# Kernel optimization log

Measured on AMD Instinct MI355X. Metric: run time of the kernel, lower is better.

The kernel has to match this reference:

```python
import jax, jax.numpy as jnp
import numpy as np

NUM_CHANNELS = 256
NUM_HEADS = 8
HEAD_DIM = NUM_CHANNELS // NUM_HEADS


def setup_inputs() -> dict:
    key = jax.random.key(0)
    k1, k2, k3, k4, k5 = jax.random.split(key, 5)
    C = NUM_CHANNELS
    s = 1.0 / np.sqrt(C)
    image = jax.random.normal(k1, (8, C, 32, 32), dtype=jnp.float32)
    # kqv_projection: Linear(C, 3C); mix_heads: Linear(C, C). Stored as [in, out].
    w_kqv = jax.random.uniform(k2, (C, 3 * C), minval=-s, maxval=s, dtype=jnp.float32)
    b_kqv = jax.random.uniform(k3, (3 * C,), minval=-s, maxval=s, dtype=jnp.float32)
    w_mix = jax.random.uniform(k4, (C, C), minval=-s, maxval=s, dtype=jnp.float32)
    b_mix = jax.random.uniform(k5, (C,), minval=-s, maxval=s, dtype=jnp.float32)
    return {"image": image, "w_kqv": w_kqv, "b_kqv": b_kqv, "w_mix": w_mix, "b_mix": b_mix}


def _masked_attention(seq, w_kqv, b_kqv, w_mix, b_mix):
    # seq: [N, T, C]
    N, T, C = seq.shape
    H, D = NUM_HEADS, HEAD_DIM
    projected = seq @ w_kqv + b_kqv            # [N, T, 3C]
    k, q, v = jnp.split(projected, 3, axis=-1)  # order: keys, queries, values
    # split heads -> [N, H, T, D]
    k = k.reshape(N, T, H, D).transpose(0, 2, 1, 3)
    q = q.reshape(N, T, H, D).transpose(0, 2, 1, 3)
    v = v.reshape(N, T, H, D).transpose(0, 2, 1, 3)
    logits = jnp.einsum('nhtd,nhsd->nhts', q, k) / jnp.sqrt(jnp.float32(D))
    causal = jnp.tril(jnp.ones((T, T), dtype=bool))
    logits = jnp.where(causal, logits, -jnp.inf)
    weights = jax.nn.softmax(logits, axis=-1)
    out = jnp.einsum('nhts,nhsd->nhtd', weights, v)  # [N, H, T, D]
    out = out.transpose(0, 2, 1, 3).reshape(N, T, C)  # combine heads
    return out @ w_mix + b_mix


def reference(image, w_kqv, b_kqv, w_mix, b_mix):
    N, C, Hh, Ww = image.shape
    seq = image.transpose(0, 2, 3, 1).reshape(N, Hh * Ww, C)
    attn = _masked_attention(seq, w_kqv, b_kqv, w_mix, b_mix)
    attn = attn.reshape(N, Hh, Ww, C).transpose(0, 3, 1, 2)
    return attn + image
```

## Files before the change

kernel.cpp:

```cpp
#include <hip/hip_runtime.h>
#include <math.h>

constexpr int NB  = 8;
constexpr int C   = 256;
constexpr int T   = 1024;
constexpr int NH  = 8;
constexpr int HD  = 32;
constexpr int C3  = 768;

constexpr float QSCALE = 0.25503489422229562f;

typedef __attribute__((ext_vector_type(8))) short bf16x8;
typedef __attribute__((ext_vector_type(4))) float f32x4;

__device__ inline short f2bf(float f) {
    unsigned u = __float_as_uint(f);
    u += 0x7FFF + ((u >> 16) & 1);
    return (short)(u >> 16);
}
__device__ inline short f2bf_trunc(float f) {
    return (short)(__float_as_uint(f) >> 16);
}

__global__ __launch_bounds__(256) void kqv_mfma(const float* __restrict__ image,
                                                const float* __restrict__ wkqv,
                                                const float* __restrict__ bkqv,
                                                short* __restrict__ Kb,
                                                short* __restrict__ Qb,
                                                short* __restrict__ Vtb) {
    __shared__ __align__(16) short As[128][40];
    __shared__ __align__(16) short Bs[64][40];
    const int tid = threadIdx.x;
    const int n0 = blockIdx.x * 64;
    const int m0 = blockIdx.y * 128;
    const int nb = m0 >> 10, t0 = m0 & 1023;
    const int wv = tid >> 6, lane = tid & 63;
    const int m = lane & 15, quad = lane >> 4;
    const int am = tid & 63, ak8 = (tid >> 6) * 8;

    const float* imgn = image + (size_t)nb * C * T;

    f32x4 acc[2][4];
    const f32x4 z = {0.f, 0.f, 0.f, 0.f};
    #pragma unroll
    for (int i = 0; i < 2; ++i)
        #pragma unroll
        for (int j = 0; j < 4; ++j) acc[i][j] = z;

    float fa[2][8], fb[8];
    #pragma unroll
    for (int i = 0; i < 8; ++i) {
        fa[0][i] = imgn[(size_t)(ak8 + i) * T + t0 + am];
        fa[1][i] = imgn[(size_t)(ak8 + i) * T + t0 + 64 + am];
        fb[i]    = wkqv[(size_t)(ak8 + i) * C3 + n0 + am];
    }

    for (int k0 = 0; k0 < C; k0 += 32) {
        __syncthreads();
        #pragma unroll
        for (int h2 = 0; h2 < 2; ++h2) {
            short4 lo = { f2bf(fa[h2][0]), f2bf(fa[h2][1]), f2bf(fa[h2][2]), f2bf(fa[h2][3]) };
            short4 hi = { f2bf(fa[h2][4]), f2bf(fa[h2][5]), f2bf(fa[h2][6]), f2bf(fa[h2][7]) };
            *(short4*)&As[64 * h2 + am][ak8]     = lo;
            *(short4*)&As[64 * h2 + am][ak8 + 4] = hi;
        }
        {
            short4 lo = { f2bf(fb[0]), f2bf(fb[1]), f2bf(fb[2]), f2bf(fb[3]) };
            short4 hi = { f2bf(fb[4]), f2bf(fb[5]), f2bf(fb[6]), f2bf(fb[7]) };
            *(short4*)&Bs[am][ak8]     = lo;
            *(short4*)&Bs[am][ak8 + 4] = hi;
        }
        if (k0 + 32 < C) {
            #pragma unroll
            for (int i = 0; i < 8; ++i) {
                fa[0][i] = imgn[(size_t)(k0 + 32 + ak8 + i) * T + t0 + am];
                fa[1][i] = imgn[(size_t)(k0 + 32 + ak8 + i) * T + t0 + 64 + am];
                fb[i]    = wkqv[(size_t)(k0 + 32 + ak8 + i) * C3 + n0 + am];
            }
        }
        __syncthreads();
        bf16x8 a[2], b[4];
        #pragma unroll
        for (int i = 0; i < 2; ++i) a[i] = *(const bf16x8*)&As[32 * wv + 16 * i + m][8 * quad];
        #pragma unroll
        for (int j = 0; j < 4; ++j) b[j] = *(const bf16x8*)&Bs[16 * j + m][8 * quad];
        #pragma unroll
        for (int i = 0; i < 2; ++i)
            #pragma unroll
            for (int j = 0; j < 4; ++j)
                acc[i][j] = __builtin_amdgcn_mfma_f32_16x16x32_bf16(a[i], b[j], acc[i][j], 0, 0, 0);
    }

    #pragma unroll
    for (int j = 0; j < 4; ++j) {
        int jj = n0 + 16 * j + m;
        int chunk = jj >> 8, hh = (jj >> 5) & 7, d = jj & 31;
        float bias = bkqv[jj];
        if (chunk < 2) {
            short* dst = (chunk == 0) ? Kb : Qb;
            float mul = (chunk == 1) ? QSCALE : 1.0f;
            size_t base = (size_t)(nb * NH + hh) * T * HD + d;
            #pragma unroll
            for (int i = 0; i < 2; ++i) {
                int t = t0 + 32 * wv + 16 * i + 4 * quad;
                #pragma unroll
                for (int r = 0; r < 4; ++r)
                    dst[base + (size_t)(t + r) * HD] = f2bf((acc[i][j][r] + bias) * mul);
            }
        } else {
            size_t base = (size_t)(nb * NH + hh) * (16 * 2048) + (size_t)d * 64;
            #pragma unroll
            for (int i = 0; i < 2; ++i) {
                #pragma unroll
                for (int r = 0; r < 4; ++r) {
                    int t = t0 + 32 * wv + 16 * i + 4 * quad + r;
                    Vtb[base + (size_t)(t >> 6) * 2048 + (t & 63)] = f2bf(acc[i][j][r] + bias);
                }
            }
        }
    }
}

__global__ __launch_bounds__(256) void attn_mfma(const short* __restrict__ Kb,
                                                 const short* __restrict__ Qb,
                                                 const short* __restrict__ Vtb,
                                                 short* __restrict__ attnb) {
    const int qb = (blockIdx.z & 4) ? 7 - blockIdx.x : blockIdx.x;
    const int h  = blockIdx.y;
    const int nb = blockIdx.z;
    const int tid  = threadIdx.x;
    const int wv   = tid >> 6;
    const int lane = tid & 63;
    const int m    = lane & 15;
    const int quad = lane >> 4;

    __shared__ __align__(16) short Ps[128][72];

    const int q0  = qb * 128;
    const int nst = 2 * qb + 2;
    const size_t hb = (size_t)(nb * NH + h) * T * HD;
    const short* Kp = Kb + hb;
    const short* Qp = Qb + hb;
    const short* Vp = Vtb + (size_t)(nb * NH + h) * (16 * 2048);
    const f32x4 z = {0.f, 0.f, 0.f, 0.f};

    bf16x8 aq[2];
    #pragma unroll
    for (int i = 0; i < 2; ++i)
        aq[i] = *(const bf16x8*)&Qp[(size_t)(q0 + 32 * wv + 16 * i + m) * HD + 8 * quad];

    bf16x8 bk[4], vb[2][2];
    #pragma unroll
    for (int j = 0; j < 4; ++j)
        bk[j] = *(const bf16x8*)&Kp[(size_t)(16 * j + m) * HD + 8 * quad];
    #pragma unroll
    for (int kc = 0; kc < 2; ++kc)
        #pragma unroll
        for (int hf = 0; hf < 2; ++hf)
            vb[kc][hf] = *(const bf16x8*)&Vp[(size_t)(16 * hf + m) * 64 + 32 * kc + 8 * quad];

    f32x4 O[2][2] = {{z, z}, {z, z}};
    float lp[2][4] = {};

    for (int st = 0; st < nst; ++st) {
        f32x4 S[2][4];
        #pragma unroll
        for (int i = 0; i < 2; ++i)
            #pragma unroll
            for (int j = 0; j < 4; ++j)
                S[i][j] = __builtin_amdgcn_mfma_f32_16x16x32_bf16(aq[i], bk[j], z, 0, 0, 0);

        if (st + 1 < nst) {
            #pragma unroll
            for (int j = 0; j < 4; ++j)
                bk[j] = *(const bf16x8*)&Kp[(size_t)((st + 1) * 64 + 16 * j + m) * HD + 8 * quad];
        }

        const bool msk = (st >= 2 * qb);
        const int s0 = st * 64;
        #pragma unroll
        for (int i = 0; i < 2; ++i) {
            const int qr_base = q0 + 32 * wv + 16 * i + 4 * quad;
            #pragma unroll
            for (int j = 0; j < 4; ++j) {
                const int sc = s0 + 16 * j + m;
                #pragma unroll
                for (int r = 0; r < 4; ++r) {
                    float e = __builtin_amdgcn_exp2f(S[i][j][r]);
                    if (msk && sc > qr_base + r) e = 0.f;
                    lp[i][r] += e;
                    Ps[32 * wv + 16 * i + 4 * quad + r][16 * j + m] = f2bf_trunc(e);
                }
            }
        }

        #pragma unroll
        for (int kc = 0; kc < 2; ++kc) {
            bf16x8 ap0 = *(const bf16x8*)&Ps[32 * wv + m][32 * kc + 8 * quad];
            bf16x8 ap1 = *(const bf16x8*)&Ps[32 * wv + 16 + m][32 * kc + 8 * quad];
            O[0][0] = __builtin_amdgcn_mfma_f32_16x16x32_bf16(ap0, vb[kc][0], O[0][0], 0, 0, 0);
            O[0][1] = __builtin_amdgcn_mfma_f32_16x16x32_bf16(ap0, vb[kc][1], O[0][1], 0, 0, 0);
            O[1][0] = __builtin_amdgcn_mfma_f32_16x16x32_bf16(ap1, vb[kc][0], O[1][0], 0, 0, 0);
            O[1][1] = __builtin_amdgcn_mfma_f32_16x16x32_bf16(ap1, vb[kc][1], O[1][1], 0, 0, 0);
        }

        if (st + 1 < nst) {
            const short* Vn = Vp + (size_t)(st + 1) * 2048;
            #pragma unroll
            for (int kc = 0; kc < 2; ++kc)
                #pragma unroll
                for (int hf = 0; hf < 2; ++hf)
                    vb[kc][hf] = *(const bf16x8*)&Vn[(size_t)(16 * hf + m) * 64 + 32 * kc + 8 * quad];
        }
    }

    #pragma unroll
    for (int i = 0; i < 2; ++i)
        #pragma unroll
        for (int r = 0; r < 4; ++r) {
            float l = lp[i][r];
            l += __shfl_xor(l, 1);
            l += __shfl_xor(l, 2);
            l += __shfl_xor(l, 4);
            l += __shfl_xor(l, 8);
            float inv = 1.f / l;
            int row = q0 + 32 * wv + 16 * i + 4 * quad + r;
            short* op = attnb + ((size_t)(nb * T + row)) * C + h * HD;
            op[m]      = f2bf(O[i][0][r] * inv);
            op[16 + m] = f2bf(O[i][1][r] * inv);
        }
}

__global__ __launch_bounds__(256) void mix_mfma(const short* __restrict__ attnb,
                                                const float* __restrict__ wmix,
                                                const float* __restrict__ bmix,
                                                const float* __restrict__ image,
                                                float* __restrict__ out) {
    __shared__ __align__(16) short Bs[64][264];
    const int tid = threadIdx.x;
    const int n0 = blockIdx.x * 64;
    const int m0 = blockIdx.y * 64;
    const int nb = m0 >> 10, t0 = m0 & 1023;
    const int wv = tid >> 6, lane = tid & 63;
    const int m = lane & 15, quad = lane >> 4;
    const int bn = tid & 63, bk8 = (tid >> 6) * 8;

    #pragma unroll
    for (int g = 0; g < 8; ++g) {
        int kk = bk8 + 32 * g;
        float fb[8];
        #pragma unroll
        for (int i = 0; i < 8; ++i)
            fb[i] = wmix[(size_t)(kk + i) * C + n0 + bn];
        short4 lo = { f2bf(fb[0]), f2bf(fb[1]), f2bf(fb[2]), f2bf(fb[3]) };
        short4 hi = { f2bf(fb[4]), f2bf(fb[5]), f2bf(fb[6]), f2bf(fb[7]) };
        *(short4*)&Bs[bn][kk]     = lo;
        *(short4*)&Bs[bn][kk + 4] = hi;
    }
    __syncthreads();

    f32x4 acc[4];
    const f32x4 z = {0.f, 0.f, 0.f, 0.f};
    #pragma unroll
    for (int j = 0; j < 4; ++j) acc[j] = z;

    #pragma unroll
    for (int k0 = 0; k0 < C; k0 += 32) {
        bf16x8 a = *(const bf16x8*)&attnb[(size_t)(m0 + 16 * wv + m) * C + k0 + 8 * quad];
        bf16x8 b[4];
        #pragma unroll
        for (int j = 0; j < 4; ++j) b[j] = *(const bf16x8*)&Bs[16 * j + m][k0 + 8 * quad];
        #pragma unroll
        for (int j = 0; j < 4; ++j)
            acc[j] = __builtin_amdgcn_mfma_f32_16x16x32_bf16(a, b[j], acc[j], 0, 0, 0);
    }

    const int tb = t0 + 16 * wv + 4 * quad;
    #pragma unroll
    for (int j = 0; j < 4; ++j) {
        int c = n0 + 16 * j + m;
        float bias = bmix[c];
        size_t o = (size_t)(nb * C + c) * T + tb;
        float4 img = *(const float4*)&image[o];
        float4 res = { acc[j][0] + bias + img.x,
                       acc[j][1] + bias + img.y,
                       acc[j][2] + bias + img.z,
                       acc[j][3] + bias + img.w };
        *(float4*)&out[o] = res;
    }
}

extern "C" void kernel_launch(void* const* d_in, const int* in_sizes, int n_in,
                              void* d_out, int out_size, void* d_ws, size_t ws_size,
                              hipStream_t stream) {
    const float* image = (const float*)d_in[0];
    const float* w_kqv = (const float*)d_in[1];
    const float* b_kqv = (const float*)d_in[2];
    const float* w_mix = (const float*)d_in[3];
    const float* b_mix = (const float*)d_in[4];
    float* out = (float*)d_out;

    short* Kb    = (short*)d_ws;
    short* Qb    = Kb  + (size_t)NB * NH * T * HD;
    short* Vtb   = Qb  + (size_t)NB * NH * T * HD;
    short* attnb = Vtb + (size_t)NB * NH * T * HD;

    kqv_mfma<<<dim3(C3 / 64, NB * T / 128), 256, 0, stream>>>(image, w_kqv, b_kqv, Kb, Qb, Vtb);
    attn_mfma<<<dim3(8, NH, NB), 256, 0, stream>>>(Kb, Qb, Vtb, attnb);
    mix_mfma<<<dim3(C / 64, NB * T / 64), 256, 0, stream>>>(attnb, w_mix, b_mix, image, out);
}
```

Measured before the change: 109.2 us.

## Pretranspose inputs to bf16 and use direct global-to-LDS loads in KQV GEMM

Adds a prep kernel that transposes the image and both weight matrices once and converts them to bf16. The KQV GEMM then streams 64-wide K tiles through global_load_lds into XOR-swizzled shared memory, and the mix GEMM copies pre-converted weights instead of converting them in every block. The attention loop is split so that only the last two diagonal tiles evaluate the causal mask. In exchange there is an extra launch plus an extra round trip of the image through memory, and the new KQV loop has no software prefetch.

```diff
diff --git a/kernel.cpp b/kernel.cpp
--- a/kernel.cpp
+++ b/kernel.cpp
@@ -22,23 +22,75 @@
     return (short)(__float_as_uint(f) >> 16);
 }
 
-__global__ __launch_bounds__(256) void kqv_mfma(const float* __restrict__ image,
-                                                const float* __restrict__ wkqv,
+__device__ __forceinline__ void gl16(const void* g, void* l) {
+    __builtin_amdgcn_global_load_lds(
+        (const __attribute__((address_space(1))) unsigned int*)g,
+        (__attribute__((address_space(3))) unsigned int*)l, 16, 0, 0);
+}
+
+__global__ __launch_bounds__(256) void prep_tc(const float* __restrict__ image,
+                                               const float* __restrict__ wkqv,
+                                               const float* __restrict__ wmix,
+                                               short* __restrict__ Xb,
+                                               short* __restrict__ Wkb,
+                                               short* __restrict__ Wmb) {
+    __shared__ float tile[64][65];
+    const int bid = blockIdx.x;
+    const int tid = threadIdx.x;
+    const float* src; short* dst;
+    int Cc, r0, c0;
+    if (bid < 512) {
+        const int nb = bid >> 6, t = bid & 63;
+        src = image + (size_t)nb * C * T;
+        dst = Xb + (size_t)nb * T * C;
+        Cc = T; r0 = (t & 3) * 64; c0 = (t >> 2) * 64;
+    } else if (bid < 560) {
+        const int t = bid - 512;
+        src = wkqv; dst = Wkb;
+        Cc = C3; r0 = (t & 3) * 64; c0 = (t >> 2) * 64;
+    } else {
+        const int t = bid - 560;
+        src = wmix; dst = Wmb;
+        Cc = C; r0 = (t & 3) * 64; c0 = (t >> 2) * 64;
+    }
+    const int lr = tid >> 4, lc = (tid & 15) * 4;
+    #pragma unroll
+    for (int p = 0; p < 4; ++p) {
+        float4 v = *(const float4*)&src[(size_t)(r0 + 16 * p + lr) * Cc + c0 + lc];
+        tile[16 * p + lr][lc + 0] = v.x;
+        tile[16 * p + lr][lc + 1] = v.y;
+        tile[16 * p + lr][lc + 2] = v.z;
+        tile[16 * p + lr][lc + 3] = v.w;
+    }
+    __syncthreads();
+    const int wc = tid >> 2, wr = (tid & 3) * 16;
+    bf16x8 v0, v1;
+    #pragma unroll
+    for (int e = 0; e < 8; ++e) v0[e] = f2bf(tile[wr + e][wc]);
+    #pragma unroll
+    for (int e = 0; e < 8; ++e) v1[e] = f2bf(tile[wr + 8 + e][wc]);
+    short* o = dst + (size_t)(c0 + wc) * C + r0 + wr;
+    *(bf16x8*)&o[0] = v0;
+    *(bf16x8*)&o[8] = v1;
+}
+
+__global__ __launch_bounds__(256) void kqv_mfma(const short* __restrict__ Xb,
+                                                const short* __restrict__ Wkb,
                                                 const float* __restrict__ bkqv,
                                                 short* __restrict__ Kb,
                                                 short* __restrict__ Qb,
                                                 short* __restrict__ Vtb) {
-    __shared__ __align__(16) short As[128][40];
-    __shared__ __align__(16) short Bs[64][40];
+    __shared__ __align__(16) short As[128 * 64];
+    __shared__ __align__(16) short Bs[64 * 64];
     const int tid = threadIdx.x;
     const int n0 = blockIdx.x * 64;
     const int m0 = blockIdx.y * 128;
     const int nb = m0 >> 10, t0 = m0 & 1023;
     const int wv = tid >> 6, lane = tid & 63;
     const int m = lane & 15, quad = lane >> 4;
-    const int am = tid & 63, ak8 = (tid >> 6) * 8;
-
-    const float* imgn = image + (size_t)nb * C * T;
+
+    const short* Xn = Xb + (size_t)nb * T * C + (size_t)t0 * C;
+    const short* Wn = Wkb + (size_t)n0 * C;
 
     f32x4 acc[2][4];
     const f32x4 z = {0.f, 0.f, 0.f, 0.f};
@@ -47,48 +99,45 @@
         #pragma unroll
         for (int j = 0; j < 4; ++j) acc[i][j] = z;
 
-    float fa[2][8], fb[8];
-    #pragma unroll
-    for (int i = 0; i < 8; ++i) {
-        fa[0][i] = imgn[(size_t)(ak8 + i) * T + t0 + am];
-        fa[1][i] = imgn[(size_t)(ak8 + i) * T + t0 + 64 + am];
-        fb[i]    = wkqv[(size_t)(ak8 + i) * C3 + n0 + am];
-    }
-
-    for (int k0 = 0; k0 < C; k0 += 32) {
+    const int sx = (m & 7) << 4;
+
+    for (int k0 = 0; k0 < C; k0 += 64) {
+        #pragma unroll
+        for (int p = 0; p < 4; ++p) {
+            const int o = p * 4096 + tid * 16;
+            const int row = o >> 7;
+            const int cb = (o & 127) ^ ((row & 7) << 4);
+            gl16(Xn + (size_t)row * C + k0 + (cb >> 1), (char*)As + o);
+        }
+        #pragma unroll
+        for (int p = 0; p < 2; ++p) {
+            const int o = p * 4096 + tid * 16;
+            const int row = o >> 7;
+            const int cb = (o & 127) ^ ((row & 7) << 4);
+            gl16(Wn + (size_t)row * C + k0 + (cb >> 1), (char*)Bs + o);
+        }
         __syncthreads();
-        #pragma unroll
-        for (int h2 = 0; h2 < 2; ++h2) {
-            short4 lo = { f2bf(fa[h2][0]), f2bf(fa[h2][1]), f2bf(fa[h2][2]), f2bf(fa[h2][3]) };
-            short4 hi = { f2bf(fa[h2][4]), f2bf(fa[h2][5]), f2bf(fa[h2][6]), f2bf(fa[h2][7]) };
-            *(short4*)&As[64 * h2 + am][ak8]     = lo;
-            *(short4*)&As[64 * h2 + am][ak8 + 4] = hi;
-        }
-        {
-            short4 lo = { f2bf(fb[0]), f2bf(fb[1]), f2bf(fb[2]), f2bf(fb[3]) };
-            short4 hi = { f2bf(fb[4]), f2bf(fb[5]), f2bf(fb[6]), f2bf(fb[7]) };
-            *(short4*)&Bs[am][ak8]     = lo;
-            *(short4*)&Bs[am][ak8 + 4] = hi;
-        }
-        if (k0 + 32 < C) {
-            #pragma unroll
-            for (int i = 0; i < 8; ++i) {
-                fa[0][i] = imgn[(size_t)(k0 + 32 + ak8 + i) * T + t0 + am];
-                fa[1][i] = imgn[(size_t)(k0 + 32 + ak8 + i) * T + t0 + 64 + am];
-                fb[i]    = wkqv[(size_t)(k0 + 32 + ak8 + i) * C3 + n0 + am];
-            }
-        }
+
+        bf16x8 a[2][2], b[2][4];
+        #pragma unroll
+        for (int kk = 0; kk < 2; ++kk) {
+            #pragma unroll
+            for (int i = 0; i < 2; ++i)
+                a[kk][i] = *(const bf16x8*)((const char*)As +
+                            (32 * wv + 16 * i + m) * 128 + ((kk * 64 + quad * 16) ^ sx));
+            #pragma unroll
+            for (int j = 0; j < 4; ++j)
+                b[kk][j] = *(const bf16x8*)((const char*)Bs +
+                            (16 * j + m) * 128 + ((kk * 64 + quad * 16) ^ sx));
+        }
+        #pragma unroll
+        for (int kk = 0; kk < 2; ++kk)
+            #pragma unroll
+            for (int i = 0; i < 2; ++i)
+                #pragma unroll
+                for (int j = 0; j < 4; ++j)
+                    acc[i][j] = __builtin_amdgcn_mfma_f32_16x16x32_bf16(a[kk][i], b[kk][j], acc[i][j], 0, 0, 0);
         __syncthreads();
-        bf16x8 a[2], b[4];
-        #pragma unroll
-        for (int i = 0; i < 2; ++i) a[i] = *(const bf16x8*)&As[32 * wv + 16 * i + m][8 * quad];
-        #pragma unroll
-        for (int j = 0; j < 4; ++j) b[j] = *(const bf16x8*)&Bs[16 * j + m][8 * quad];
-        #pragma unroll
-        for (int i = 0; i < 2; ++i)
-            #pragma unroll
-            for (int j = 0; j < 4; ++j)
-                acc[i][j] = __builtin_amdgcn_mfma_f32_16x16x32_bf16(a[i], b[j], acc[i][j], 0, 0, 0);
     }
 
     #pragma unroll
@@ -162,7 +211,7 @@
     f32x4 O[2][2] = {{z, z}, {z, z}};
     float lp[2][4] = {};
 
-    for (int st = 0; st < nst; ++st) {
+    auto step = [&](const int st, const bool msk) {
         f32x4 S[2][4];
         #pragma unroll
         for (int i = 0; i < 2; ++i)
@@ -176,7 +225,6 @@
                 bk[j] = *(const bf16x8*)&Kp[(size_t)((st + 1) * 64 + 16 * j + m) * HD + 8 * quad];
         }
 
-        const bool msk = (st >= 2 * qb);
         const int s0 = st * 64;
         #pragma unroll
         for (int i = 0; i < 2; ++i) {
@@ -212,7 +260,12 @@
                 for (int hf = 0; hf < 2; ++hf)
                     vb[kc][hf] = *(const bf16x8*)&Vn[(size_t)(16 * hf + m) * 64 + 32 * kc + 8 * quad];
         }
-    }
+    };
+
+    const int mq = 2 * qb;
+    for (int st = 0; st < mq; ++st) step(st, false);
+    step(mq, true);
+    step(mq + 1, true);
 
     #pragma unroll
     for (int i = 0; i < 2; ++i)
@@ -232,7 +285,7 @@
 }
 
 __global__ __launch_bounds__(256) void mix_mfma(const short* __restrict__ attnb,
-                                                const float* __restrict__ wmix,
+                                                const short* __restrict__ Wmb,
                                                 const float* __restrict__ bmix,
                                                 const float* __restrict__ image,
                                                 float* __restrict__ out) {
@@ -243,19 +296,13 @@
     const int nb = m0 >> 10, t0 = m0 & 1023;
     const int wv = tid >> 6, lane = tid & 63;
     const int m = lane & 15, quad = lane >> 4;
-    const int bn = tid & 63, bk8 = (tid >> 6) * 8;
-
-    #pragma unroll
-    for (int g = 0; g < 8; ++g) {
-        int kk = bk8 + 32 * g;
-        float fb[8];
-        #pragma unroll
-        for (int i = 0; i < 8; ++i)
-            fb[i] = wmix[(size_t)(kk + i) * C + n0 + bn];
-        short4 lo = { f2bf(fb[0]), f2bf(fb[1]), f2bf(fb[2]), f2bf(fb[3]) };
-        short4 hi = { f2bf(fb[4]), f2bf(fb[5]), f2bf(fb[6]), f2bf(fb[7]) };
-        *(short4*)&Bs[bn][kk]     = lo;
-        *(short4*)&Bs[bn][kk + 4] = hi;
+
+    {
+        const short* wrow = Wmb + (size_t)(n0 + (tid >> 2)) * C + (tid & 3) * 64;
+        short* brow = &Bs[tid >> 2][(tid & 3) * 64];
+        #pragma unroll
+        for (int g = 0; g < 8; ++g)
+            *(bf16x8*)&brow[8 * g] = *(const bf16x8*)&wrow[8 * g];
     }
     __syncthreads();
 
@@ -300,12 +347,16 @@
     const float* b_mix = (const float*)d_in[4];
     float* out = (float*)d_out;
 
-    short* Kb    = (short*)d_ws;
+    short* Xb    = (short*)d_ws;
+    short* Wkb   = Xb  + (size_t)NB * T * C;
+    short* Wmb   = Wkb + (size_t)C3 * C;
+    short* Kb    = Wmb + (size_t)C * C;
     short* Qb    = Kb  + (size_t)NB * NH * T * HD;
     short* Vtb   = Qb  + (size_t)NB * NH * T * HD;
     short* attnb = Vtb + (size_t)NB * NH * T * HD;
 
-    kqv_mfma<<<dim3(C3 / 64, NB * T / 128), 256, 0, stream>>>(image, w_kqv, b_kqv, Kb, Qb, Vtb);
+    prep_tc<<<576, 256, 0, stream>>>(image, w_kqv, w_mix, Xb, Wkb, Wmb);
+    kqv_mfma<<<dim3(C3 / 64, NB * T / 128), 256, 0, stream>>>(Xb, Wkb, b_kqv, Kb, Qb, Vtb);
     attn_mfma<<<dim3(8, NH, NB), 256, 0, stream>>>(Kb, Qb, Vtb, attnb);
-    mix_mfma<<<dim3(C / 64, NB * T / 64), 256, 0, stream>>>(attnb, w_mix, b_mix, image, out);
-}
+    mix_mfma<<<dim3(C / 64, NB * T / 64), 256, 0, stream>>>(attnb, Wmb, b_mix, image, out);
+}
```

Measured after the change: 105.1 us. 1.04x faster.
